# Kernel optimization log

Measured on AMD Instinct MI355X. Metric: run time of the kernel, lower is better.

The kernel has to match this reference:

```python
import jax, jax.numpy as jnp
import numpy as np

A, B, O, ACT, H, NH = 16, 8192, 128, 16, 128, 4
D = H // NH  # attend_dim
IN = O + ACT
NEG = -1e9


def setup_inputs() -> dict:
    key = jax.random.key(0)
    ks = jax.random.split(key, 16)
    s = lambda k, shape, fan: jax.random.normal(k, shape, jnp.float32) / np.sqrt(fan)
    return {
        "obs": jax.random.normal(ks[0], (A, B, O), jnp.float32),
        "actions": jax.random.uniform(ks[1], (A, B, ACT), jnp.float32),
        # per-agent sa-encoder (enc_fc1)
        "W_sa": s(ks[2], (A, IN, H), IN), "b_sa": jnp.zeros((A, H), jnp.float32),
        # per-agent state encoder (s_enc_fc1)
        "W_s": s(ks[3], (A, O, H), O), "b_s": jnp.zeros((A, H), jnp.float32),
        # shared per-head extractors
        "Wk": s(ks[4], (NH, H, D), H),
        "Wsel": s(ks[5], (NH, H, D), H),
        "Wv": s(ks[6], (NH, H, D), H), "bv": jnp.zeros((NH, D), jnp.float32),
        # per-agent critic MLP
        "Wc1": s(ks[7], (A, 2 * H, H), 2 * H), "bc1": jnp.zeros((A, H), jnp.float32),
        "Wc2": s(ks[8], (A, H, ACT), H), "bc2": jnp.zeros((A, ACT), jnp.float32),
    }


def _bn(x):
    # BatchNorm1d(affine=False) in training mode: normalize over batch axis, biased var
    m = x.mean(axis=1, keepdims=True)
    v = x.var(axis=1, keepdims=True)
    return (x - m) / jnp.sqrt(v + 1e-5)


def reference(obs, actions, W_sa, b_sa, W_s, b_s, Wk, Wsel, Wv, bv, Wc1, bc1, Wc2, bc2):
    lrelu = jax.nn.leaky_relu  # slope 0.01, matches torch default
    inp = jnp.concatenate([obs, actions], axis=-1)            # [A,B,IN]
    sa = lrelu(jnp.einsum('abi,aih->abh', _bn(inp), W_sa) + b_sa[:, None, :])  # [A,B,H]
    se = lrelu(jnp.einsum('abo,aoh->abh', _bn(obs), W_s) + b_s[:, None, :])    # [A,B,H]
    keys = jnp.einsum('abh,nhd->nabd', sa, Wk)                # [NH,A,B,D]
    vals = lrelu(jnp.einsum('abh,nhd->nabd', sa, Wv) + bv[:, None, None, :])
    sel = jnp.einsum('abh,nhd->nabd', se, Wsel)
    logits = jnp.einsum('nibd,njbd->nibj', sel, keys) / np.sqrt(D)  # [NH,A,B,A]
    self_mask = jnp.eye(A, dtype=bool)[None, :, None, :]      # mask j == i
    w = jax.nn.softmax(jnp.where(self_mask, NEG, logits), axis=-1)
    other = jnp.einsum('nibj,njbd->nibd', w, vals)            # [NH,A,B,D]
    other = jnp.transpose(other, (1, 2, 0, 3)).reshape(A, B, NH * D)  # head-order concat
    cin = jnp.concatenate([se, other], axis=-1)               # [A,B,2H]
    h = lrelu(jnp.einsum('abk,akh->abh', cin, Wc1) + bc1[:, None, :])
    all_q = jnp.einsum('abh,aho->abo', h, Wc2) + bc2[:, None, :]      # [A,B,ACT]
    idx = jnp.argmax(actions, axis=-1)[..., None]             # int_acs, [A,B,1]
    q = jnp.take_along_axis(all_q, idx, axis=-1)              # [A,B,1]
    return q
```

## Files before the change

### kernel.cpp

```cpp
#include <hip/hip_runtime.h>
#include <hip/hip_bf16.h>

#define A_N 16
#define B_N 8192
#define O_N 128
#define ACT_N 16
#define H_N 128
#define NH_N 4
#define D_N 32
#define IN_N 144
#define NEGV -1e9f

typedef __attribute__((ext_vector_type(8))) short short8;
typedef __attribute__((ext_vector_type(4))) float floatx4;

static __device__ inline unsigned short f2bf(float f) {
    union { float f; unsigned u; } x{f};
    unsigned u = x.u + 0x7FFFu + ((x.u >> 16) & 1u);
    return (unsigned short)(u >> 16);
}
static __device__ inline unsigned pack_bf2(float a, float b) {
    union { float f; unsigned u; } xa{a}, xb{b};
    unsigned ua = xa.u + 0x7FFFu + ((xa.u >> 16) & 1u);
    unsigned ub = xb.u + 0x7FFFu + ((xb.u >> 16) & 1u);
    return (ua >> 16) | (ub & 0xFFFF0000u);
}
static __device__ inline float bf2f(unsigned short h) {
    union { unsigned u; float f; } x;
    x.u = ((unsigned)h) << 16;
    return x.f;
}
static __device__ inline float bflo(unsigned u) {
    union { unsigned u; float f; } x; x.u = u << 16; return x.f;
}
static __device__ inline float bfhi(unsigned u) {
    union { unsigned u; float f; } x; x.u = u & 0xFFFF0000u; return x.f;
}
static __device__ inline short8 ld_frag(const unsigned* p) {
    union { unsigned u[4]; short8 v; } x;
    uint2 lo = *(const uint2*)p;
    uint2 hi = *(const uint2*)(p + 2);
    x.u[0] = lo.x; x.u[1] = lo.y; x.u[2] = hi.x; x.u[3] = hi.y;
    return x.v;
}
static __device__ inline short8 ld_frag4(const unsigned* p) {
    union { uint4 q; short8 v; } x;
    x.q = *(const uint4*)p;
    return x.v;
}
static __device__ inline short8 mk_frag(unsigned a, unsigned b, unsigned c, unsigned d) {
    union { unsigned u[4]; short8 v; } x;
    x.u[0] = a; x.u[1] = b; x.u[2] = c; x.u[3] = d;
    return x.v;
}

__global__ __launch_bounds__(256) void k_stats(const float* __restrict__ obs,
                                               const float* __restrict__ act,
                                               float* __restrict__ gsumP,
                                               float* __restrict__ gsqP) {
    __shared__ float ssum[IN_N];
    __shared__ float ssq[IN_N];
    int a = blockIdx.x >> 4;
    int slab = blockIdx.x & 15;
    int r0 = slab * 512;
    int t = threadIdx.x;
    if (t < IN_N) { ssum[t] = 0.f; ssq[t] = 0.f; }
    __syncthreads();
    {
        int c0 = (t & 31) * 4, rg = t >> 5;
        const float* p = obs + ((size_t)a * B_N + r0 + rg) * O_N + c0;
        float s0 = 0.f, s1 = 0.f, s2 = 0.f, s3 = 0.f;
        float q0 = 0.f, q1 = 0.f, q2 = 0.f, q3 = 0.f;
#pragma unroll 4
        for (int i = 0; i < 64; ++i) {
            float4 v = *(const float4*)(p + (size_t)i * 8 * O_N);
            s0 += v.x; q0 += v.x * v.x;
            s1 += v.y; q1 += v.y * v.y;
            s2 += v.z; q2 += v.z * v.z;
            s3 += v.w; q3 += v.w * v.w;
        }
        atomicAdd(&ssum[c0 + 0], s0); atomicAdd(&ssq[c0 + 0], q0);
        atomicAdd(&ssum[c0 + 1], s1); atomicAdd(&ssq[c0 + 1], q1);
        atomicAdd(&ssum[c0 + 2], s2); atomicAdd(&ssq[c0 + 2], q2);
        atomicAdd(&ssum[c0 + 3], s3); atomicAdd(&ssq[c0 + 3], q3);
    }
    if (t < 128) {
        int f = t & 15, rg = t >> 4;
        const float* p = act + ((size_t)a * B_N + r0 + rg) * ACT_N + f;
        float s = 0.f, q = 0.f;
#pragma unroll 4
        for (int i = 0; i < 64; ++i) {
            float v = p[(size_t)i * 8 * ACT_N];
            s += v; q += v * v;
        }
        atomicAdd(&ssum[O_N + f], s);
        atomicAdd(&ssq[O_N + f], q);
    }
    __syncthreads();
    if (t < IN_N) {
        gsumP[(a * 16 + slab) * IN_N + t] = ssum[t];
        gsqP[(a * 16 + slab) * IN_N + t] = ssq[t];
    }
}

__global__ __launch_bounds__(256) void k_finalize(const float* __restrict__ gsumP,
                                                  const float* __restrict__ gsqP,
                                                  float* __restrict__ mean,
                                                  float* __restrict__ rstd) {
    int i = blockIdx.x * 256 + threadIdx.x;
    if (i < A_N * IN_N) {
        int a = i / IN_N, f = i - a * IN_N;
        float s = 0.f, q = 0.f;
#pragma unroll
        for (int sl = 0; sl < 16; ++sl) {
            s += gsumP[(a * 16 + sl) * IN_N + f];
            q += gsqP[(a * 16 + sl) * IN_N + f];
        }
        const float invB = 1.f / (float)B_N;
        float m = s * invB;
        float v = fmaxf(q * invB - m * m, 0.f);
        mean[i] = m;
        rstd[i] = rsqrtf(v + 1e-5f);
    }
}

#define L1E 393216
#define P1E 409600
#define P2E 417792
#define CRE 679936
#define C2E 712704
#define BFE (C2E + 4096)
__global__ __launch_bounds__(256) void k_wprep(
    const float* __restrict__ W_sa, const float* __restrict__ W_s,
    const float* __restrict__ Wk, const float* __restrict__ Wsel,
    const float* __restrict__ Wv, const float* __restrict__ Wc1,
    const float* __restrict__ Wc2, const float* __restrict__ mean,
    const float* __restrict__ rstd,
    const float* __restrict__ b_sa, const float* __restrict__ b_s,
    unsigned* __restrict__ wt_l1, unsigned* __restrict__ wt_p1,
    unsigned* __restrict__ wt_p2, unsigned* __restrict__ wt_cr,
    float* __restrict__ wt_c2, float* __restrict__ fb) {
    int idx = blockIdx.x * 256 + threadIdx.x;
    if (idx < L1E) {
        int a = idx / 24576, rem = idx % 24576;
        int n = rem & 255, kp = rem >> 8;
        int k0 = 2 * kp, k1 = k0 + 1;
        float v0 = 0.f, v1 = 0.f;
        if (n < 128) {
            if (k0 < IN_N) v0 = W_sa[((size_t)a * IN_N + k0) * H_N + n] * rstd[a * IN_N + k0];
            if (k1 < IN_N) v1 = W_sa[((size_t)a * IN_N + k1) * H_N + n] * rstd[a * IN_N + k1];
        } else {
            int m = n - 128;
            if (k0 < O_N) v0 = W_s[((size_t)a * O_N + k0) * H_N + m] * rstd[a * IN_N + k0];
            if (k1 < O_N) v1 = W_s[((size_t)a * O_N + k1) * H_N + m] * rstd[a * IN_N + k1];
        }
        wt_l1[(size_t)a * 24576 + n * 96 + kp] = pack_bf2(v0, v1);
    } else if (idx < P1E) {
        int i2 = idx - L1E;
        int n = i2 & 255, kp = i2 >> 8;
        int k0 = 2 * kp;
        float v0, v1;
        if (n < 128) {
            const float* w = Wk + ((size_t)(n >> 5) * H_N) * D_N + (n & 31);
            v0 = w[(size_t)k0 * D_N]; v1 = w[(size_t)(k0 + 1) * D_N];
        } else {
            int m = n - 128;
            const float* w = Wv + ((size_t)(m >> 5) * H_N) * D_N + (m & 31);
            v0 = w[(size_t)k0 * D_N]; v1 = w[(size_t)(k0 + 1) * D_N];
        }
        wt_p1[n * 64 + kp] = pack_bf2(v0, v1);
    } else if (idx < P2E) {
        int i3 = idx - P1E;
        int n = i3 & 127, kp = i3 >> 7;
        int k0 = 2 * kp;
        const float* w = Wsel + ((size_t)(n >> 5) * H_N) * D_N + (n & 31);
        wt_p2[n * 64 + kp] = pack_bf2(w[(size_t)k0 * D_N], w[(size_t)(k0 + 1) * D_N]);
    } else if (idx < CRE) {
        int i4 = idx - P2E;
        int a = i4 >> 14, r = i4 & 16383;
        int n = r & 127, kp = r >> 7;
        int k0 = 2 * kp;
        const float* w = Wc1 + (size_t)a * 256 * H_N + n;
        wt_cr[(size_t)a * 16384 + n * 128 + kp] =
            pack_bf2(w[(size_t)k0 * H_N], w[(size_t)(k0 + 1) * H_N]);
    } else if (idx < C2E) {
        int i5 = idx - CRE;
        int a = i5 >> 11, rem = i5 & 2047;
        int oo = rem >> 7, h = rem & 127;
        wt_c2[i5] = Wc2[((size_t)a * H_N + h) * ACT_N + oo];
    } else if (idx < BFE) {
        int i6 = idx - C2E;
        int a = i6 >> 8, c = i6 & 255;
        float s = 0.f;
        if (c < 128) {
            for (int k = 0; k < IN_N; ++k)
                s += mean[a * IN_N + k] * rstd[a * IN_N + k] *
                     W_sa[((size_t)a * IN_N + k) * H_N + c];
            fb[a * 128 + c] = b_sa[a * H_N + c] - s;
        } else {
            int m = c - 128;
            for (int k = 0; k < O_N; ++k)
                s += mean[a * IN_N + k] * rstd[a * IN_N + k] *
                     W_s[((size_t)a * O_N + k) * H_N + m];
            fb[2048 + a * 128 + m] = b_s[a * H_N + m] - s;
        }
    }
}

__global__ __launch_bounds__(512, 2) void k_l1(
    const float* __restrict__ obs, const float* __restrict__ act,
    const unsigned* __restrict__ wt_l1, const float* __restrict__ fb,
    unsigned short* __restrict__ sa_us, unsigned short* __restrict__ se_us,
    int b0g, int Bc) {
    __shared__ unsigned smem[(128 + 256) * 34];
    unsigned* Xs = smem;
    unsigned* Ws = smem + 128 * 34;

    int a = blockIdx.y;
    int b0 = blockIdx.x * 128;
    int t = threadIdx.x;
    int wid = t >> 6, lane = t & 63, lm = lane & 15, lq = lane >> 4;
    int wrow = (wid & 1) * 64;
    int wcol = (wid >> 1) * 64;

    floatx4 acc[4][4];
#pragma unroll
    for (int mt = 0; mt < 4; ++mt)
#pragma unroll
        for (int nt = 0; nt < 4; ++nt)
#pragma unroll
            for (int e = 0; e < 4; ++e) acc[mt][nt][e] = 0.f;

    const unsigned* WtA = wt_l1 + (size_t)a * 24576;

    for (int c = 0; c < 3; ++c) {
        int kk = c * 64;
        __syncthreads();
        for (int idx = t; idx < 128 * 16; idx += 512) {
            int r = idx >> 4, c4 = idx & 15;
            int k = kk + c4 * 4;
            size_t grow = (size_t)a * B_N + b0g + b0 + r;
            float4 v;
            if (k < O_N) v = *(const float4*)&obs[grow * O_N + k];
            else if (k < IN_N) v = *(const float4*)&act[grow * ACT_N + (k - O_N)];
            else v = make_float4(0.f, 0.f, 0.f, 0.f);
            uint2* dst = (uint2*)&Xs[r * 34 + c4 * 2];
            *dst = make_uint2(pack_bf2(v.x, v.y), pack_bf2(v.z, v.w));
        }
        for (int idx = t; idx < 256 * 8; idx += 512) {
            int n = idx >> 3, c4 = idx & 7;
            uint4 w = *(const uint4*)&WtA[(size_t)n * 96 + (kk >> 1) + c4 * 4];
            uint2* dst = (uint2*)&Ws[n * 34 + c4 * 4];
            dst[0] = make_uint2(w.x, w.y);
            dst[1] = make_uint2(w.z, w.w);
        }
        __syncthreads();
#pragma unroll
        for (int s = 0; s < 2; ++s) {
            if (kk + s * 32 >= 160) break;
            short8 afr[4];
#pragma unroll
            for (int mt = 0; mt < 4; ++mt)
                afr[mt] = ld_frag(&Xs[(wrow + mt * 16 + lm) * 34 + s * 16 + lq * 4]);
#pragma unroll
            for (int nt = 0; nt < 4; ++nt) {
                short8 bfr = ld_frag(&Ws[(wcol + nt * 16 + lm) * 34 + s * 16 + lq * 4]);
#pragma unroll
                for (int mt = 0; mt < 4; ++mt)
                    acc[mt][nt] = __builtin_amdgcn_mfma_f32_16x16x32_bf16(
                        afr[mt], bfr, acc[mt][nt], 0, 0, 0);
            }
        }
    }

    int zsel = (wcol >= 128);
    unsigned short* outp = zsel ? se_us : sa_us;
    const float* bias = fb + zsel * 2048 + a * 128;
    int cbase = wcol & 127;
#pragma unroll
    for (int mt = 0; mt < 4; ++mt)
#pragma unroll
        for (int nt = 0; nt < 4; ++nt)
#pragma unroll
            for (int r = 0; r < 4; ++r) {
                int row = wrow + mt * 16 + lq * 4 + r;
                int col = cbase + nt * 16 + lm;
                float v = acc[mt][nt][r] + bias[col];
                v = v > 0.f ? v : 0.01f * v;
                outp[((size_t)(b0 + row) * 16 + a) * 128 + col] = f2bf(v);
            }
}

__global__ __launch_bounds__(256, 3) void k_fused(
    const unsigned* __restrict__ sa_u, const unsigned* __restrict__ se_u,
    const unsigned* __restrict__ wt_p1, const unsigned* __restrict__ wt_p2,
    const float* __restrict__ bv, unsigned short* __restrict__ other_us,
    int Bc) {
    __shared__ unsigned Xs[64 * 66];
    __shared__ unsigned short keys_s[64 * 130];
    __shared__ unsigned short valsT[4 * 128 * 20];
    unsigned short* sel_s = (unsigned short*)Xs;

    int bg0 = blockIdx.x * 4;
    int t = threadIdx.x;
    int wid = t >> 6, lane = t & 63, lm = lane & 15, lq = lane >> 4;

    const unsigned* sa_base = sa_u + (size_t)(bg0 * 16) * 64;
    const unsigned* se_base = se_u + (size_t)(bg0 * 16) * 64;

    for (int idx = t; idx < 64 * 16; idx += 256) {
        int r = idx >> 4, c4 = idx & 15;
        uint4 v = *(const uint4*)&sa_base[(size_t)idx * 4];
        uint2* dst = (uint2*)&Xs[r * 66 + c4 * 4];
        dst[0] = make_uint2(v.x, v.y);
        dst[1] = make_uint2(v.z, v.w);
    }
    uint4 seR[4];
#pragma unroll
    for (int ii = 0; ii < 4; ++ii)
        seR[ii] = *(const uint4*)&se_base[(size_t)(t + ii * 256) * 4];
    __syncthreads();

    {
        floatx4 acc[4][4];
#pragma unroll
        for (int mt = 0; mt < 4; ++mt)
#pragma unroll
            for (int nt = 0; nt < 4; ++nt)
#pragma unroll
                for (int e = 0; e < 4; ++e) acc[mt][nt][e] = 0.f;
#pragma unroll
        for (int s = 0; s < 4; ++s) {
            short8 afr[4];
#pragma unroll
            for (int mt = 0; mt < 4; ++mt)
                afr[mt] = ld_frag(&Xs[(mt * 16 + lm) * 66 + s * 16 + lq * 4]);
#pragma unroll
            for (int nt = 0; nt < 4; ++nt) {
                int col = wid * 64 + nt * 16 + lm;
                short8 bfr = ld_frag4(wt_p1 + (size_t)col * 64 + s * 16 + lq * 4);
#pragma unroll
                for (int mt = 0; mt < 4; ++mt)
                    acc[mt][nt] = __builtin_amdgcn_mfma_f32_16x16x32_bf16(
                        afr[mt], bfr, acc[mt][nt], 0, 0, 0);
            }
        }
        if (wid < 2) {
#pragma unroll
            for (int mt = 0; mt < 4; ++mt)
#pragma unroll
                for (int nt = 0; nt < 4; ++nt)
#pragma unroll
                    for (int r = 0; r < 4; ++r) {
                        int row = mt * 16 + lq * 4 + r;
                        int col = wid * 64 + nt * 16 + lm;
                        keys_s[row * 130 + col] = f2bf(acc[mt][nt][r]);
                    }
        } else {
#pragma unroll
            for (int mt = 0; mt < 4; ++mt)
#pragma unroll
                for (int nt = 0; nt < 4; ++nt) {
                    int d = (wid - 2) * 64 + nt * 16 + lm;
                    float bvc = bv[d];
                    float v0 = acc[mt][nt][0] + bvc; v0 = v0 > 0.f ? v0 : 0.01f * v0;
                    float v1 = acc[mt][nt][1] + bvc; v1 = v1 > 0.f ? v1 : 0.01f * v1;
                    float v2 = acc[mt][nt][2] + bvc; v2 = v2 > 0.f ? v2 : 0.01f * v2;
                    float v3 = acc[mt][nt][3] + bvc; v3 = v3 > 0.f ? v3 : 0.01f * v3;
                    uint2 o = make_uint2(pack_bf2(v0, v1), pack_bf2(v2, v3));
                    *(uint2*)&valsT[mt * 2560 + d * 20 + lq * 4] = o;
                }
        }
    }
    __syncthreads();

#pragma unroll
    for (int ii = 0; ii < 4; ++ii) {
        int idx = t + ii * 256;
        int r = idx >> 4, c4 = idx & 15;
        uint2* dst = (uint2*)&Xs[r * 66 + c4 * 4];
        dst[0] = make_uint2(seR[ii].x, seR[ii].y);
        dst[1] = make_uint2(seR[ii].z, seR[ii].w);
    }
    __syncthreads();

    {
        int wcol = wid * 32;
        floatx4 acc[4][2];
#pragma unroll
        for (int mt = 0; mt < 4; ++mt)
#pragma unroll
            for (int nt = 0; nt < 2; ++nt)
#pragma unroll
                for (int e = 0; e < 4; ++e) acc[mt][nt][e] = 0.f;
#pragma unroll
        for (int s = 0; s < 4; ++s) {
            short8 afr[4];
#pragma unroll
            for (int mt = 0; mt < 4; ++mt)
                afr[mt] = ld_frag(&Xs[(mt * 16 + lm) * 66 + s * 16 + lq * 4]);
#pragma unroll
            for (int nt = 0; nt < 2; ++nt) {
                int col = wcol + nt * 16 + lm;
                short8 bfr = ld_frag4(wt_p2 + (size_t)col * 64 + s * 16 + lq * 4);
#pragma unroll
                for (int mt = 0; mt < 4; ++mt)
                    acc[mt][nt] = __builtin_amdgcn_mfma_f32_16x16x32_bf16(
                        afr[mt], bfr, acc[mt][nt], 0, 0, 0);
            }
        }
        __syncthreads();
#pragma unroll
        for (int mt = 0; mt < 4; ++mt)
#pragma unroll
            for (int nt = 0; nt < 2; ++nt)
#pragma unroll
                for (int r = 0; r < 4; ++r) {
                    int row = mt * 16 + lq * 4 + r;
                    int col = wcol + nt * 16 + lm;
                    sel_s[row * 132 + col] = f2bf(acc[mt][nt][r]);
                }
    }
    __syncthreads();

    const unsigned* selU = (const unsigned*)sel_s;
    const unsigned* keysU = (const unsigned*)keys_s;
    int bsub = wid;
    floatx4 lgacc[4];
#pragma unroll
    for (int n = 0; n < 4; ++n) {
        short8 af = ld_frag(&keysU[(bsub * 16 + lm) * 65 + n * 16 + lq * 4]);
        short8 bf = ld_frag(&selU[(bsub * 16 + lm) * 66 + n * 16 + lq * 4]);
        floatx4 z4 = {0.f, 0.f, 0.f, 0.f};
        lgacc[n] = __builtin_amdgcn_mfma_f32_16x16x32_bf16(af, bf, z4, 0, 0, 0);
    }

    const float scale = 0.17677669529663687f;
    int dr = lm - lq * 4;
    unsigned pq0[4], pq1[4];
#pragma unroll
    for (int n = 0; n < 4; ++n) {
        float p0 = lgacc[n][0] * scale;
        float p1 = lgacc[n][1] * scale;
        float p2 = lgacc[n][2] * scale;
        float p3 = lgacc[n][3] * scale;
        if (dr == 0) p0 = NEGV;
        if (dr == 1) p1 = NEGV;
        if (dr == 2) p2 = NEGV;
        if (dr == 3) p3 = NEGV;
        float m = fmaxf(fmaxf(p0, p1), fmaxf(p2, p3));
        m = fmaxf(m, __shfl_xor(m, 16));
        m = fmaxf(m, __shfl_xor(m, 32));
        p0 = __expf(p0 - m); p1 = __expf(p1 - m);
        p2 = __expf(p2 - m); p3 = __expf(p3 - m);
        float s = p0 + p1 + p2 + p3;
        s += __shfl_xor(s, 16);
        s += __shfl_xor(s, 32);
        float inv = 1.f / s;
        pq0[n] = pack_bf2(p0 * inv, p1 * inv);
        pq1[n] = pack_bf2(p2 * inv, p3 * inv);
    }

    const unsigned* valsTU = (const unsigned*)valsT;
    int g = lq & 1;
    int s0l = (g << 5) + lm;
    int s1l = s0l + 16;
    size_t obase = ((size_t)(bg0 + bsub) * 16 + lm) * 128;
#pragma unroll
    for (int n = 0; n < 4; ++n) {
        unsigned b0 = __shfl(pq0[n], s0l);
        unsigned b1 = __shfl(pq1[n], s0l);
        unsigned b2 = __shfl(pq0[n], s1l);
        unsigned b3 = __shfl(pq1[n], s1l);
        if (lq >= 2) { b0 = 0u; b1 = 0u; b2 = 0u; b3 = 0u; }
        short8 bfr = mk_frag(b0, b1, b2, b3);
#pragma unroll
        for (int dt = 0; dt < 2; ++dt) {
            int d = n * 32 + dt * 16 + lm;
            const unsigned* vrow = valsTU + (bsub * 1280 + d * 10 + (g << 2));
            uint2 av0 = *(const uint2*)vrow;
            uint2 av1 = *(const uint2*)(vrow + 2);
            unsigned a0 = av0.x, a1 = av0.y, a2 = av1.x, a3 = av1.y;
            if (lq >= 2) { a0 = 0u; a1 = 0u; a2 = 0u; a3 = 0u; }
            short8 afr = mk_frag(a0, a1, a2, a3);
            floatx4 z4 = {0.f, 0.f, 0.f, 0.f};
            floatx4 c = __builtin_amdgcn_mfma_f32_16x16x32_bf16(afr, bfr, z4, 0, 0, 0);
            uint2 o = make_uint2(pack_bf2(c[0], c[1]), pack_bf2(c[2], c[3]));
            *(uint2*)&other_us[obase + n * 32 + dt * 16 + lq * 4] = o;
        }
    }
}

__global__ __launch_bounds__(256, 4) void k_critic(
    const unsigned* __restrict__ se_u, const unsigned* __restrict__ other_u,
    const unsigned* __restrict__ wt_cr,
    const float* __restrict__ bc1, const float* __restrict__ actions,
    const float* __restrict__ wt_c2, const float* __restrict__ bc2,
    float* __restrict__ qout, int b0g, int Bc) {
    __shared__ unsigned smem[(64 + 128) * 34];
    unsigned* Xs = smem;
    unsigned* Ws = smem + 64 * 34;

    int a = blockIdx.y;
    int b0 = blockIdx.x * 64;
    int t = threadIdx.x;
    int wid = t >> 6, lane = t & 63, lm = lane & 15, lq = lane >> 4;
    int wrow = (wid & 1) * 32;
    int wcol = (wid >> 1) * 64;

    floatx4 acc[2][4];
#pragma unroll
    for (int mt = 0; mt < 2; ++mt)
#pragma unroll
        for (int nt = 0; nt < 4; ++nt)
#pragma unroll
            for (int e = 0; e < 4; ++e) acc[mt][nt][e] = 0.f;

    const unsigned* WtA = wt_cr + (size_t)a * 16384;

    for (int c = 0; c < 4; ++c) {
        int kk = c * 64;
        __syncthreads();
        const unsigned* src = (c < 2) ? se_u : other_u;
        int off = (c & 1) * 32;
        for (int idx = t; idx < 64 * 8; idx += 256) {
            int r = idx >> 3, c4 = idx & 7;
            uint4 v = *(const uint4*)&src[((size_t)(b0 + r) * 16 + a) * 64 + off + c4 * 4];
            uint2* dst = (uint2*)&Xs[r * 34 + c4 * 4];
            dst[0] = make_uint2(v.x, v.y);
            dst[1] = make_uint2(v.z, v.w);
        }
        for (int idx = t; idx < 128 * 8; idx += 256) {
            int n = idx >> 3, c4 = idx & 7;
            uint4 w = *(const uint4*)&WtA[(size_t)n * 128 + (kk >> 1) + c4 * 4];
            uint2* dst = (uint2*)&Ws[n * 34 + c4 * 4];
            dst[0] = make_uint2(w.x, w.y);
            dst[1] = make_uint2(w.z, w.w);
        }
        __syncthreads();
#pragma unroll
        for (int s = 0; s < 2; ++s) {
            short8 afr[2];
#pragma unroll
            for (int mt = 0; mt < 2; ++mt)
                afr[mt] = ld_frag(&Xs[(wrow + mt * 16 + lm) * 34 + s * 16 + lq * 4]);
#pragma unroll
            for (int nt = 0; nt < 4; ++nt) {
                short8 bfr = ld_frag(&Ws[(wcol + nt * 16 + lm) * 34 + s * 16 + lq * 4]);
#pragma unroll
                for (int mt = 0; mt < 2; ++mt)
                    acc[mt][nt] = __builtin_amdgcn_mfma_f32_16x16x32_bf16(
                        afr[mt], bfr, acc[mt][nt], 0, 0, 0);
            }
        }
    }

    __syncthreads();
    unsigned short* hbuf = (unsigned short*)smem;
#pragma unroll
    for (int mt = 0; mt < 2; ++mt)
#pragma unroll
        for (int nt = 0; nt < 4; ++nt)
#pragma unroll
            for (int r = 0; r < 4; ++r) {
                int row = wrow + mt * 16 + lq * 4 + r;
                int col = wcol + nt * 16 + lm;
                float v = acc[mt][nt][r] + bc1[a * H_N + col];
                v = v > 0.f ? v : 0.01f * v;
                hbuf[row * 132 + col] = f2bf(v);
            }
    __syncthreads();
    if (t < 64) {
        size_t arow = (size_t)a * B_N + b0g + b0 + t;
        const float* ap = &actions[arow * ACT_N];
        float bestv = ap[0];
        int bi = 0;
        for (int o = 1; o < ACT_N; ++o) {
            float v = ap[o];
            if (v > bestv) { bestv = v; bi = o; }
        }
        float q = bc2[a * ACT_N + bi];
        const float4* w4p = (const float4*)&wt_c2[((size_t)a * ACT_N + bi) * H_N];
        const uint2* hp2 = (const uint2*)&hbuf[t * 132];
#pragma unroll
        for (int h4 = 0; h4 < 32; ++h4) {
            float4 w4 = w4p[h4];
            uint2 hh = hp2[h4];
            q = fmaf(bflo(hh.x), w4.x, q);
            q = fmaf(bfhi(hh.x), w4.y, q);
            q = fmaf(bflo(hh.y), w4.z, q);
            q = fmaf(bfhi(hh.y), w4.w, q);
        }
        qout[arow] = q;
    }
}

extern "C" void kernel_launch(void* const* d_in, const int* in_sizes, int n_in,
                              void* d_out, int out_size, void* d_ws, size_t ws_size,
                              hipStream_t stream) {
    const float* obs     = (const float*)d_in[0];
    const float* actions = (const float*)d_in[1];
    const float* W_sa    = (const float*)d_in[2];
    const float* b_sa    = (const float*)d_in[3];
    const float* W_s     = (const float*)d_in[4];
    const float* b_s     = (const float*)d_in[5];
    const float* Wk      = (const float*)d_in[6];
    const float* Wsel    = (const float*)d_in[7];
    const float* Wv      = (const float*)d_in[8];
    const float* bv      = (const float*)d_in[9];
    const float* Wc1     = (const float*)d_in[10];
    const float* bc1     = (const float*)d_in[11];
    const float* Wc2     = (const float*)d_in[12];
    const float* bc2     = (const float*)d_in[13];
    float* out = (float*)d_out;
    char* ws = (char*)d_ws;

    size_t o = 0;
    float* gsumP = (float*)(ws + o); o += (size_t)36864 * 4;
    float* gsqP  = (float*)(ws + o); o += (size_t)36864 * 4;
    float* meanA = (float*)(ws + o); o += 2304 * 4;
    float* rstdA = (float*)(ws + o); o += 2304 * 4;
    unsigned* wt_l1 = (unsigned*)(ws + o); o += (size_t)393216 * 4;
    unsigned* wt_p1 = (unsigned*)(ws + o); o += (size_t)16384 * 4;
    unsigned* wt_p2 = (unsigned*)(ws + o); o += (size_t)8192 * 4;
    unsigned* wt_cr = (unsigned*)(ws + o); o += (size_t)262144 * 4;
    float* fb = (float*)(ws + o); o += (size_t)4096 * 4;
    float* wt_c2 = (float*)(ws + o); o += (size_t)32768 * 4;
    size_t fixed = o;

    int Bc = B_N;
    while (Bc > 128 && fixed + 12288ull * Bc > ws_size) Bc >>= 1;

    unsigned short* sa_us = (unsigned short*)(ws + o); o += (size_t)A_N * Bc * 128 * 2;
    unsigned short* se_us = (unsigned short*)(ws + o); o += (size_t)A_N * Bc * 128 * 2;
    unsigned short* ot_us = (unsigned short*)(ws + o); o += (size_t)A_N * Bc * 128 * 2;

    k_stats<<<dim3(A_N * 16), 256, 0, stream>>>(obs, actions, gsumP, gsqP);
    k_finalize<<<dim3(9), 256, 0, stream>>>(gsumP, gsqP, meanA, rstdA);
    k_wprep<<<dim3(BFE / 256), 256, 0, stream>>>(W_sa, W_s, Wk, Wsel, Wv, Wc1, Wc2,
                                                 meanA, rstdA, b_sa, b_s,
                                                 wt_l1, wt_p1, wt_p2, wt_cr, wt_c2, fb);

    for (int b0g = 0; b0g < B_N; b0g += Bc) {
        k_l1<<<dim3(Bc / 128, A_N), 512, 0, stream>>>(
            obs, actions, wt_l1, fb, sa_us, se_us, b0g, Bc);
        k_fused<<<dim3(Bc / 4), 256, 0, stream>>>(
            (const unsigned*)sa_us, (const unsigned*)se_us, wt_p1, wt_p2, bv,
            ot_us, Bc);
        k_critic<<<dim3(Bc / 64, A_N), 256, 0, stream>>>(
            (const unsigned*)se_us, (const unsigned*)ot_us, wt_cr, bc1,
            actions, wt_c2, bc2, out, b0g, Bc);
    }
}
```

Before: 268.8 us.

## Merge keys/vals and sel projections into one MFMA phase with double LDS buffer

Loads both sa and se tiles into two separate LDS buffers at once, then computes the keys, vals and sel projections in a single MFMA loop in which each wave holds 24 accumulator tiles. This removes one LDS staging pass and one or two block barriers, and rebalances the work so every wave does both keys/vals columns and sel columns. In exchange it raises LDS and register use, and launch bounds drop from 3 to 2 blocks per CU, which lowers occupancy.

```diff
diff --git a/kernel.cpp b/kernel.cpp
--- a/kernel.cpp
+++ b/kernel.cpp
@@ -291,15 +291,15 @@
             }
 }
 
-__global__ __launch_bounds__(256, 3) void k_fused(
+__global__ __launch_bounds__(256, 2) void k_fused(
     const unsigned* __restrict__ sa_u, const unsigned* __restrict__ se_u,
     const unsigned* __restrict__ wt_p1, const unsigned* __restrict__ wt_p2,
     const float* __restrict__ bv, unsigned short* __restrict__ other_us,
     int Bc) {
-    __shared__ unsigned Xs[64 * 66];
+    __shared__ unsigned Xs[2][64 * 66];
     __shared__ unsigned short keys_s[64 * 130];
     __shared__ unsigned short valsT[4 * 128 * 20];
-    unsigned short* sel_s = (unsigned short*)Xs;
+    unsigned short* sel_s = (unsigned short*)&Xs[0][0];
 
     int bg0 = blockIdx.x * 4;
     int t = threadIdx.x;
@@ -311,116 +311,85 @@
     for (int idx = t; idx < 64 * 16; idx += 256) {
         int r = idx >> 4, c4 = idx & 15;
         uint4 v = *(const uint4*)&sa_base[(size_t)idx * 4];
-        uint2* dst = (uint2*)&Xs[r * 66 + c4 * 4];
-        dst[0] = make_uint2(v.x, v.y);
-        dst[1] = make_uint2(v.z, v.w);
-    }
-    uint4 seR[4];
-#pragma unroll
-    for (int ii = 0; ii < 4; ++ii)
-        seR[ii] = *(const uint4*)&se_base[(size_t)(t + ii * 256) * 4];
+        uint4 w = *(const uint4*)&se_base[(size_t)idx * 4];
+        uint2* d0 = (uint2*)&Xs[0][r * 66 + c4 * 4];
+        d0[0] = make_uint2(v.x, v.y);
+        d0[1] = make_uint2(v.z, v.w);
+        uint2* d1 = (uint2*)&Xs[1][r * 66 + c4 * 4];
+        d1[0] = make_uint2(w.x, w.y);
+        d1[1] = make_uint2(w.z, w.w);
+    }
     __syncthreads();
 
-    {
-        floatx4 acc[4][4];
+    floatx4 acc[4][6];
+#pragma unroll
+    for (int mt = 0; mt < 4; ++mt)
+#pragma unroll
+        for (int nt = 0; nt < 6; ++nt)
+#pragma unroll
+            for (int e = 0; e < 4; ++e) acc[mt][nt][e] = 0.f;
+#pragma unroll
+    for (int s = 0; s < 4; ++s) {
+        short8 sfr[4], efr[4];
 #pragma unroll
         for (int mt = 0; mt < 4; ++mt)
-#pragma unroll
-            for (int nt = 0; nt < 4; ++nt)
-#pragma unroll
-                for (int e = 0; e < 4; ++e) acc[mt][nt][e] = 0.f;
-#pragma unroll
-        for (int s = 0; s < 4; ++s) {
-            short8 afr[4];
+            sfr[mt] = ld_frag(&Xs[0][(mt * 16 + lm) * 66 + s * 16 + lq * 4]);
+#pragma unroll
+        for (int mt = 0; mt < 4; ++mt)
+            efr[mt] = ld_frag(&Xs[1][(mt * 16 + lm) * 66 + s * 16 + lq * 4]);
+#pragma unroll
+        for (int nt = 0; nt < 4; ++nt) {
+            int col = wid * 32 + (nt & 1) * 16 + lm + ((nt >= 2) ? 128 : 0);
+            short8 bfr = ld_frag4(wt_p1 + (size_t)col * 64 + s * 16 + lq * 4);
 #pragma unroll
             for (int mt = 0; mt < 4; ++mt)
-                afr[mt] = ld_frag(&Xs[(mt * 16 + lm) * 66 + s * 16 + lq * 4]);
-#pragma unroll
-            for (int nt = 0; nt < 4; ++nt) {
-                int col = wid * 64 + nt * 16 + lm;
-                short8 bfr = ld_frag4(wt_p1 + (size_t)col * 64 + s * 16 + lq * 4);
-#pragma unroll
-                for (int mt = 0; mt < 4; ++mt)
-                    acc[mt][nt] = __builtin_amdgcn_mfma_f32_16x16x32_bf16(
-                        afr[mt], bfr, acc[mt][nt], 0, 0, 0);
-            }
-        }
-        if (wid < 2) {
+                acc[mt][nt] = __builtin_amdgcn_mfma_f32_16x16x32_bf16(
+                    sfr[mt], bfr, acc[mt][nt], 0, 0, 0);
+        }
+#pragma unroll
+        for (int nt = 4; nt < 6; ++nt) {
+            int col = wid * 32 + (nt - 4) * 16 + lm;
+            short8 bfr = ld_frag4(wt_p2 + (size_t)col * 64 + s * 16 + lq * 4);
 #pragma unroll
             for (int mt = 0; mt < 4; ++mt)
-#pragma unroll
-                for (int nt = 0; nt < 4; ++nt)
-#pragma unroll
-                    for (int r = 0; r < 4; ++r) {
-                        int row = mt * 16 + lq * 4 + r;
-                        int col = wid * 64 + nt * 16 + lm;
-                        keys_s[row * 130 + col] = f2bf(acc[mt][nt][r]);
-                    }
-        } else {
-#pragma unroll
-            for (int mt = 0; mt < 4; ++mt)
-#pragma unroll
-                for (int nt = 0; nt < 4; ++nt) {
-                    int d = (wid - 2) * 64 + nt * 16 + lm;
-                    float bvc = bv[d];
-                    float v0 = acc[mt][nt][0] + bvc; v0 = v0 > 0.f ? v0 : 0.01f * v0;
-                    float v1 = acc[mt][nt][1] + bvc; v1 = v1 > 0.f ? v1 : 0.01f * v1;
-                    float v2 = acc[mt][nt][2] + bvc; v2 = v2 > 0.f ? v2 : 0.01f * v2;
-                    float v3 = acc[mt][nt][3] + bvc; v3 = v3 > 0.f ? v3 : 0.01f * v3;
-                    uint2 o = make_uint2(pack_bf2(v0, v1), pack_bf2(v2, v3));
-                    *(uint2*)&valsT[mt * 2560 + d * 20 + lq * 4] = o;
-                }
-        }
-    }
+                acc[mt][nt] = __builtin_amdgcn_mfma_f32_16x16x32_bf16(
+                    efr[mt], bfr, acc[mt][nt], 0, 0, 0);
+        }
+    }
+
+#pragma unroll
+    for (int mt = 0; mt < 4; ++mt)
+#pragma unroll
+        for (int nt = 0; nt < 2; ++nt) {
+            int col = wid * 32 + nt * 16 + lm;
+#pragma unroll
+            for (int r = 0; r < 4; ++r)
+                keys_s[(mt * 16 + lq * 4 + r) * 130 + col] = f2bf(acc[mt][nt][r]);
+        }
+#pragma unroll
+    for (int mt = 0; mt < 4; ++mt)
+#pragma unroll
+        for (int nt = 0; nt < 2; ++nt) {
+            int d = wid * 32 + nt * 16 + lm;
+            float bvc = bv[d];
+            float v0 = acc[mt][nt + 2][0] + bvc; v0 = v0 > 0.f ? v0 : 0.01f * v0;
+            float v1 = acc[mt][nt + 2][1] + bvc; v1 = v1 > 0.f ? v1 : 0.01f * v1;
+            float v2 = acc[mt][nt + 2][2] + bvc; v2 = v2 > 0.f ? v2 : 0.01f * v2;
+            float v3 = acc[mt][nt + 2][3] + bvc; v3 = v3 > 0.f ? v3 : 0.01f * v3;
+            *(uint2*)&valsT[mt * 2560 + d * 20 + lq * 4] =
+                make_uint2(pack_bf2(v0, v1), pack_bf2(v2, v3));
+        }
     __syncthreads();
 
 #pragma unroll
-    for (int ii = 0; ii < 4; ++ii) {
-        int idx = t + ii * 256;
-        int r = idx >> 4, c4 = idx & 15;
-        uint2* dst = (uint2*)&Xs[r * 66 + c4 * 4];
-        dst[0] = make_uint2(seR[ii].x, seR[ii].y);
-        dst[1] = make_uint2(seR[ii].z, seR[ii].w);
-    }
-    __syncthreads();
-
-    {
-        int wcol = wid * 32;
-        floatx4 acc[4][2];
-#pragma unroll
-        for (int mt = 0; mt < 4; ++mt)
-#pragma unroll
-            for (int nt = 0; nt < 2; ++nt)
-#pragma unroll
-                for (int e = 0; e < 4; ++e) acc[mt][nt][e] = 0.f;
-#pragma unroll
-        for (int s = 0; s < 4; ++s) {
-            short8 afr[4];
-#pragma unroll
-            for (int mt = 0; mt < 4; ++mt)
-                afr[mt] = ld_frag(&Xs[(mt * 16 + lm) * 66 + s * 16 + lq * 4]);
-#pragma unroll
-            for (int nt = 0; nt < 2; ++nt) {
-                int col = wcol + nt * 16 + lm;
-                short8 bfr = ld_frag4(wt_p2 + (size_t)col * 64 + s * 16 + lq * 4);
-#pragma unroll
-                for (int mt = 0; mt < 4; ++mt)
-                    acc[mt][nt] = __builtin_amdgcn_mfma_f32_16x16x32_bf16(
-                        afr[mt], bfr, acc[mt][nt], 0, 0, 0);
-            }
-        }
-        __syncthreads();
-#pragma unroll
-        for (int mt = 0; mt < 4; ++mt)
-#pragma unroll
-            for (int nt = 0; nt < 2; ++nt)
-#pragma unroll
-                for (int r = 0; r < 4; ++r) {
-                    int row = mt * 16 + lq * 4 + r;
-                    int col = wcol + nt * 16 + lm;
-                    sel_s[row * 132 + col] = f2bf(acc[mt][nt][r]);
-                }
-    }
+    for (int mt = 0; mt < 4; ++mt)
+#pragma unroll
+        for (int nt = 0; nt < 2; ++nt) {
+            int col = wid * 32 + nt * 16 + lm;
+#pragma unroll
+            for (int r = 0; r < 4; ++r)
+                sel_s[(mt * 16 + lq * 4 + r) * 132 + col] = f2bf(acc[mt][nt + 4][r]);
+        }
     __syncthreads();
 
     const unsigned* selU = (const unsigned*)sel_s;
```

New measurement: 269.0 us. About the same (+0.1%).
